# Kernel tuning notes

Measured on AMD Instinct MI355X. Metric: run time of the kernel, lower is better.

The kernel has to match this reference:

```python
import jax, jax.numpy as jnp
import numpy as np

EMBED = 1024
HEADS = 16
HDIM = 64
FF = 4096
N, S = 2, 2048
EPS = 1e-5


def _ln(x, g, b):
    m = jnp.mean(x, axis=-1, keepdims=True)
    v = jnp.mean((x - m) ** 2, axis=-1, keepdims=True)
    return (x - m) / jnp.sqrt(v + EPS) * g + b


def setup_inputs() -> dict:
    key = jax.random.key(0)
    ks = jax.random.split(key, 12)
    sd = 0.02
    inp = {
        'x': jax.random.normal(ks[0], (N, S, EMBED), dtype=jnp.float32),
        'mask': jnp.ones((N, 1, S, S), dtype=jnp.int32),
        'Wq': jax.random.normal(ks[1], (EMBED, HEADS * HDIM), dtype=jnp.float32) * sd,
        'bq': jnp.zeros((HEADS * HDIM,), dtype=jnp.float32),
        'Wk': jax.random.normal(ks[2], (EMBED, HEADS * HDIM), dtype=jnp.float32) * sd,
        'bk': jnp.zeros((HEADS * HDIM,), dtype=jnp.float32),
        'Wv': jax.random.normal(ks[3], (EMBED, HEADS * HDIM), dtype=jnp.float32) * sd,
        'bv': jnp.zeros((HEADS * HDIM,), dtype=jnp.float32),
        'Wo': jax.random.normal(ks[4], (HEADS * HDIM, EMBED), dtype=jnp.float32) * sd,
        'bo': jnp.zeros((EMBED,), dtype=jnp.float32),
        'g1': jnp.ones((EMBED,), dtype=jnp.float32),
        'beta1': jnp.zeros((EMBED,), dtype=jnp.float32),
        'g2': jnp.ones((EMBED,), dtype=jnp.float32),
        'beta2': jnp.zeros((EMBED,), dtype=jnp.float32),
        'W1': jax.random.normal(ks[5], (EMBED, FF), dtype=jnp.float32) * sd,
        'b1': jnp.zeros((FF,), dtype=jnp.float32),
        'W2': jax.random.normal(ks[6], (FF, EMBED), dtype=jnp.float32) * sd,
        'b2': jnp.zeros((EMBED,), dtype=jnp.float32),
    }
    return inp


def reference(x, mask, Wq, bq, Wk, bk, Wv, bv, Wo, bo, g1, beta1, g2, beta2, W1, b1, W2, b2):
    n, q_len, _ = x.shape
    # QKV projections, split into heads: [n, s, h, d]
    Q = (x @ Wq + bq).reshape(n, q_len, HEADS, HDIM)
    K = (x @ Wk + bk).reshape(n, q_len, HEADS, HDIM)
    V = (x @ Wv + bv).reshape(n, q_len, HEADS, HDIM)
    scores = jnp.einsum('nqhd,nkhd->nhqk', Q, K)
    scores = jnp.where(mask == 0, -jnp.inf, scores)
    # NOTE: original torch code is `attention / embed_size ** 1 / 2`,
    # which parses as (scores / embed_size) / 2 — replicated faithfully.
    attn = jax.nn.softmax(scores / EMBED / 2.0, axis=-1)
    ctx = jnp.einsum('nhqk,nkhd->nqhd', attn, V).reshape(n, q_len, HEADS * HDIM)
    proj = ctx @ Wo + bo
    h = _ln(proj + x, g1, beta1)  # dropout is identity (eval / p=0)
    ff = jax.nn.relu(h @ W1 + b1) @ W2 + b2
    out = _ln(ff + h, g2, beta2)
    return out
```

## Files before the change

kernel.cpp:

```cpp
#include <hip/hip_runtime.h>
#include <hip/hip_bf16.h>
#include <cstdint>
#include <cstddef>

#define EMBED 1024
#define SLEN  2048
#define NB    2
#define HEADS 16
#define HDIM  64
#define FFDIM 4096
#define ROWS  (NB * SLEN)
#define LOG2E 1.4426950408889634f

typedef __attribute__((ext_vector_type(8))) __bf16 bf16x8;
typedef __attribute__((ext_vector_type(4))) __bf16 bf16x4;
typedef __attribute__((ext_vector_type(4))) float  f32x4;

__device__ __forceinline__ void gload_lds16(const void* g, void* l) {
  __builtin_amdgcn_global_load_lds(
      (const __attribute__((address_space(1))) void*)g,
      (__attribute__((address_space(3))) void*)l, 16, 0, 0);
}

#define SCHED() __builtin_amdgcn_sched_barrier(0)
#define BAR()                              \
  do {                                     \
    __builtin_amdgcn_s_barrier();          \
    __builtin_amdgcn_sched_barrier(0);     \
  } while (0)
#define WAITVM(N)                                           \
  do {                                                      \
    asm volatile("s_waitcnt vmcnt(" #N ")" ::: "memory");   \
  } while (0)
#define WAITLGKM(N)                                         \
  do {                                                      \
    asm volatile("s_waitcnt lgkmcnt(" #N ")" ::: "memory"); \
  } while (0)

__global__ __launch_bounds__(256) void prologue_k(
    const float* __restrict__ x, const int* __restrict__ mask,
    const float* __restrict__ Wq, const float* __restrict__ Wk,
    const float* __restrict__ Wv, const float* __restrict__ Wo,
    const float* __restrict__ W1, const float* __restrict__ W2,
    __bf16* __restrict__ xb, int* __restrict__ flags,
    __bf16* __restrict__ Wqt, __bf16* __restrict__ Wkt, __bf16* __restrict__ Wvt,
    __bf16* __restrict__ Wot, __bf16* __restrict__ W1t, __bf16* __restrict__ W2t) {
  const int b = blockIdx.x;
  const int tid = threadIdx.x;
  if (b < 3072) {
    __shared__ float t[64][65];
    const float* src;
    __bf16* dst;
    int R, C, tile;
    if (b < 1024) {
      const int w = b >> 8;
      tile = b & 255; R = 1024; C = 1024;
      src = (w == 0) ? Wq : (w == 1) ? Wk : (w == 2) ? Wv : Wo;
      dst = (w == 0) ? Wqt : (w == 1) ? Wkt : (w == 2) ? Wvt : Wot;
    } else if (b < 2048) {
      tile = b - 1024; R = 1024; C = 4096; src = W1; dst = W1t;
    } else {
      tile = b - 2048; R = 4096; C = 1024; src = W2; dst = W2t;
    }
    const int ct = C >> 6;
    const int tr = (tile / ct) * 64, tc = (tile % ct) * 64;
    const int tx = tid & 63;
    const int ty = tid >> 6;
#pragma unroll
    for (int i = 0; i < 16; ++i) {
      int a = ty * 16 + i;
      t[a][tx] = src[(size_t)(tr + a) * C + tc + tx];
    }
    __syncthreads();
#pragma unroll
    for (int i = 0; i < 16; ++i) {
      int bb = ty * 16 + i;
      dst[(size_t)(tc + bb) * R + tr + tx] = (__bf16)t[tx][bb];
    }
  } else if (b < 4096) {
    const int base = (b - 3072) * 1024;
#pragma unroll
    for (int it = 0; it < 4; ++it) {
      const int i = base + it * 256 + tid;
      float4 v = ((const float4*)x)[i];
      bf16x4 o;
      o.x = (__bf16)v.x; o.y = (__bf16)v.y; o.z = (__bf16)v.z; o.w = (__bf16)v.w;
      ((bf16x4*)xb)[i] = o;
    }
  } else {
    const int mb = b - 4096;
    const int kt = mb & 31, qt = (mb >> 5) & 15, n = mb >> 9;
    const int* base = mask + ((size_t)n * SLEN + qt * 128) * SLEN + kt * 64;
    const int rw = tid >> 4;
    const int cg = tid & 15;
    int ok = 1;
#pragma unroll
    for (int i = 0; i < 8; ++i) {
      int4 v = ((const int4*)(base + (size_t)(rw + i * 16) * SLEN))[cg];
      ok &= (v.x != 0) & (v.y != 0) & (v.z != 0) & (v.w != 0);
    }
    __shared__ int red;
    if (tid == 0) red = 1;
    __syncthreads();
    if (!ok) red = 0;
    __syncthreads();
    if (tid == 0) flags[mb] = red;
  }
}

template <int MODE>
__global__ __launch_bounds__(512, 1) void gemm256(
    const __bf16* __restrict__ A, const __bf16* __restrict__ Bt,
    const float* __restrict__ bias, const float* __restrict__ bias2,
    const float* __restrict__ bias3,
    void* __restrict__ outp, void* __restrict__ outp2, void* __restrict__ outp3,
    int M, int N, int K, int Kc, float oscale) {
  __shared__ __align__(16) char smem[131072];
  const int tid = threadIdx.x;
  const int lane = tid & 63;
  const int ntile = N >> 8;
  const int mt = M >> 8;
  const int cpx = gridDim.x >> 3;
  int u = (blockIdx.x & 7) * cpx + (blockIdx.x >> 3);
  int kz = 0;
  if constexpr (MODE == 5) {
    const int tiles = mt * ntile;
    kz = u / tiles;
    u -= kz * tiles;
  }
  int bm, bn;
  {
    const int G = (ntile >= 4) ? 4 : ntile;
    const int gsz = mt * G;
    const int g = u / gsz;
    const int rem = u - g * gsz;
    bm = rem / G;
    bn = g * G + rem % G;
  }
  const int trow = bm << 8, tcol = bn << 8;

  const int r0 = tid & 255;
  const int c0 = tid >> 8;
  const __bf16* Ag = A + (size_t)(trow + r0) * K + (size_t)kz * Kc + c0 * 8;
  const __bf16* Bg = Bt + (size_t)(tcol + r0) * K + (size_t)kz * Kc + c0 * 8;

  auto stage = [&](int buf, int kt) {
    const __bf16* a0 = Ag + (size_t)kt * 32;
    const __bf16* b0 = Bg + (size_t)kt * 32;
    char* la = smem + buf * 32768 + tid * 16;
    char* lb = la + 16384;
    gload_lds16(a0, la);
    gload_lds16(a0 + 16, la + 8192);
    gload_lds16(b0, lb);
    gload_lds16(b0 + 16, lb + 8192);
  };

  const int wave = tid >> 6;
  const int wr = wave >> 2;
  const int wc = wave & 3;
  const int l16 = lane & 15;
  const int g4 = lane >> 4;

  f32x4 acc[8][4];
#pragma unroll
  for (int i = 0; i < 8; ++i)
#pragma unroll
    for (int j = 0; j < 4; ++j) acc[i][j] = (f32x4)0.0f;

  const int nk = Kc >> 5;
  stage(0, 0);
  stage(1, 1);
  stage(2, 2);
  WAITVM(8);
  BAR();
  for (int kt = 0; kt < nk; ++kt) {
    const int cur = kt & 3;
    const char* base = smem + cur * 32768;
    bf16x8 af[8], bfr[4];
#pragma unroll
    for (int i = 0; i < 4; ++i)
      af[i] = *(const bf16x8*)(base + g4 * 4096 + (wr * 128 + i * 16 + l16) * 16);
#pragma unroll
    for (int j = 0; j < 4; ++j)
      bfr[j] = *(const bf16x8*)(base + 16384 + g4 * 4096 + (wc * 64 + j * 16 + l16) * 16);
    SCHED();
#pragma unroll
    for (int i = 4; i < 8; ++i)
      af[i] = *(const bf16x8*)(base + g4 * 4096 + (wr * 128 + i * 16 + l16) * 16);
    if (kt + 3 < nk) stage((kt + 3) & 3, kt + 3);
    SCHED();
    WAITLGKM(4);
    SCHED();
    __builtin_amdgcn_s_setprio(1);
#pragma unroll
    for (int mi = 0; mi < 4; ++mi)
#pragma unroll
      for (int ni = 0; ni < 4; ++ni)
        acc[mi][ni] =
            __builtin_amdgcn_mfma_f32_16x16x32_bf16(af[mi], bfr[ni], acc[mi][ni], 0, 0, 0);
    __builtin_amdgcn_s_setprio(0);
    SCHED();
    WAITLGKM(0);
    SCHED();
    __builtin_amdgcn_s_setprio(1);
#pragma unroll
    for (int mi = 4; mi < 8; ++mi)
#pragma unroll
      for (int ni = 0; ni < 4; ++ni)
        acc[mi][ni] =
            __builtin_amdgcn_mfma_f32_16x16x32_bf16(af[mi], bfr[ni], acc[mi][ni], 0, 0, 0);
    __builtin_amdgcn_s_setprio(0);
    if (kt + 3 < nk) {
      WAITVM(8);
    } else if (kt + 3 == nk) {
      WAITVM(4);
    } else if (kt + 2 == nk) {
      WAITVM(0);
    }
    BAR();
  }

  if constexpr (MODE == 5) {
#pragma unroll
    for (int mi = 0; mi < 8; ++mi)
#pragma unroll
      for (int ni = 0; ni < 4; ++ni) {
        const int col = tcol + wc * 64 + ni * 16 + l16;
#pragma unroll
        for (int r = 0; r < 4; ++r) {
          const int row = trow + wr * 128 + mi * 16 + g4 * 4 + r;
          ((float*)outp)[(size_t)kz * M * N + (size_t)row * N + col] = acc[mi][ni][r];
        }
      }
  } else {
    const int sel = (MODE == 4) ? (tcol >> 10) : 0;
    const float* bp = (MODE == 4) ? (sel == 0 ? bias : sel == 1 ? bias2 : bias3) : bias;
    const int cc0 = (MODE == 4) ? (tcol & 1023) : tcol;
    const int n = trow >> 11;
    if (MODE == 4 && sel == 2) {
      __bf16(*repT)[136] = (__bf16(*)[136])smem;
#pragma unroll
      for (int h = 0; h < 2; ++h) {
        __syncthreads();
        if (wr == h) {
#pragma unroll
          for (int mi = 0; mi < 8; ++mi)
#pragma unroll
            for (int ni = 0; ni < 4; ++ni) {
              const int cl = wc * 64 + ni * 16 + l16;
              const float bcol = bp[cc0 + cl];
#pragma unroll
              for (int r = 0; r < 4; ++r)
                repT[cl][mi * 16 + g4 * 4 + r] = (__bf16)(acc[mi][ni][r] + bcol);
            }
        }
        __syncthreads();
#pragma unroll
        for (int it = 0; it < 8; ++it) {
          const int cidx = it * 512 + tid;
          const int cl = cidx >> 4, seg = cidx & 15;
          const int col = cc0 + cl, hh = col >> 6, dd = col & 63;
          *(bf16x8*)((__bf16*)outp3 + ((size_t)((n * HEADS + hh) * HDIM) + dd) * SLEN +
                     (trow & 2047) + h * 128 + seg * 8) = *(const bf16x8*)&repT[cl][seg * 8];
        }
      }
    } else {
      __bf16(*rep)[264] = (__bf16(*)[264])smem;
#pragma unroll
      for (int h = 0; h < 2; ++h) {
        __syncthreads();
        if (wr == h) {
#pragma unroll
          for (int mi = 0; mi < 8; ++mi)
#pragma unroll
            for (int ni = 0; ni < 4; ++ni) {
              const int cl = wc * 64 + ni * 16 + l16;
              float bcol = bp[cc0 + cl];
#pragma unroll
              for (int r = 0; r < 4; ++r) {
                float v = acc[mi][ni][r] + bcol;
                if constexpr (MODE == 4) {
                  if (sel == 0) v *= oscale;
                } else {
                  v = fmaxf(v, 0.0f);
                }
                rep[mi * 16 + g4 * 4 + r][cl] = (__bf16)v;
              }
            }
        }
        __syncthreads();
        if constexpr (MODE == 3) {
#pragma unroll
          for (int it = 0; it < 8; ++it) {
            const int cidx = it * 512 + tid;
            const int rl = cidx >> 5, seg = cidx & 31;
            *(bf16x8*)((__bf16*)outp + (size_t)(trow + h * 128 + rl) * N + tcol + seg * 8) =
                *(const bf16x8*)&rep[rl][seg * 8];
          }
        } else {
          __bf16* dst = (sel == 0) ? (__bf16*)outp : (__bf16*)outp2;
#pragma unroll
          for (int it = 0; it < 8; ++it) {
            const int cidx = it * 512 + tid;
            const int rl = cidx >> 5, seg = cidx & 31;
            const int col = cc0 + seg * 8, hh = col >> 6, d = col & 63;
            const int s = (trow & 2047) + h * 128 + rl;
            *(bf16x8*)(dst + ((size_t)((n * HEADS + hh) * SLEN) + s) * HDIM + d) =
                *(const bf16x8*)&rep[rl][seg * 8];
          }
        }
      }
    }
  }
}

__global__ __launch_bounds__(256, 2) void gemm_bt5(
    const __bf16* __restrict__ A, const __bf16* __restrict__ Bt,
    float* __restrict__ outp, int M, int N, int K, int Kc) {
  __shared__ __align__(16) char smem[65536];
  const int tid = threadIdx.x;
  const int lane = tid & 63;
  const int ntile = N >> 7;
  const int cpx = gridDim.x >> 3;
  int u = (blockIdx.x & 7) * cpx + (blockIdx.x >> 3);
  const int tiles = (M >> 7) * ntile;
  const int kz = u / tiles;
  u -= kz * tiles;
  const int bm = u / ntile;
  const int bn = u % ntile;
  const int trow = bm << 7;
  const int tcol = bn << 7;

  const int c0 = tid >> 7;
  const int r0 = tid & 127;
  const __bf16* Ag = A + (size_t)(trow + r0) * K + (size_t)kz * Kc + c0 * 8;
  const __bf16* Bg = Bt + (size_t)(tcol + r0) * K + (size_t)kz * Kc + c0 * 8;

  auto stage = [&](int buf, int kt) {
    const __bf16* a0 = Ag + (size_t)kt * 32;
    const __bf16* b0 = Bg + (size_t)kt * 32;
    char* la = smem + buf * 16384 + tid * 16;
    char* lb = la + 8192;
    gload_lds16(a0, la);
    gload_lds16(a0 + 16, la + 4096);
    gload_lds16(b0, lb);
    gload_lds16(b0 + 16, lb + 4096);
  };

  const int wave = tid >> 6;
  const int wr = (wave >> 1) * 64;
  const int wc = (wave & 1) * 64;
  const int l16 = lane & 15;
  const int g4 = lane >> 4;

  f32x4 acc[4][4];
#pragma unroll
  for (int i = 0; i < 4; ++i)
#pragma unroll
    for (int j = 0; j < 4; ++j) acc[i][j] = (f32x4)0.0f;

  const int nk = Kc >> 5;
  stage(0, 0);
  stage(1, 1);
  stage(2, 2);
  WAITVM(8);
  BAR();
  for (int kt = 0; kt < nk; ++kt) {
    const int cur = kt & 3;
    const char* base = smem + cur * 16384;
    bf16x8 af[4], bfr[4];
#pragma unroll
    for (int i = 0; i < 4; ++i) {
      af[i]  = *(const bf16x8*)(base + g4 * 2048 + (wr + i * 16 + l16) * 16);
      bfr[i] = *(const bf16x8*)(base + 8192 + g4 * 2048 + (wc + i * 16 + l16) * 16);
    }
    if (kt + 3 < nk) stage((kt + 3) & 3, kt + 3);
    SCHED();
    WAITLGKM(0);
    SCHED();
    __builtin_amdgcn_s_setprio(1);
#pragma unroll
    for (int mi = 0; mi < 4; ++mi)
#pragma unroll
      for (int ni = 0; ni < 4; ++ni)
        acc[mi][ni] =
            __builtin_amdgcn_mfma_f32_16x16x32_bf16(af[mi], bfr[ni], acc[mi][ni], 0, 0, 0);
    __builtin_amdgcn_s_setprio(0);
    if (kt + 3 < nk) {
      WAITVM(8);
    } else if (kt + 3 == nk) {
      WAITVM(4);
    } else if (kt + 2 == nk) {
      WAITVM(0);
    }
    BAR();
  }
#pragma unroll
  for (int mi = 0; mi < 4; ++mi)
#pragma unroll
    for (int ni = 0; ni < 4; ++ni) {
      const int col = tcol + wc + ni * 16 + l16;
#pragma unroll
      for (int r = 0; r < 4; ++r) {
        const int row = trow + wr + mi * 16 + g4 * 4 + r;
        outp[(size_t)kz * M * N + (size_t)row * N + col] = acc[mi][ni][r];
      }
    }
}

__global__ __launch_bounds__(256, 3) void attn_k(const __bf16* __restrict__ Q,
                                                 const __bf16* __restrict__ K,
                                                 const __bf16* __restrict__ Vt,
                                                 const int* __restrict__ mask,
                                                 const int* __restrict__ flags,
                                                 __bf16* __restrict__ ctx) {
  const int tid = threadIdx.x, lane = tid & 63, wave = tid >> 6;
  const int l16 = lane & 15, g4 = lane >> 4;
  const int bid = blockIdx.x;
  const int lb = (bid & 7) * 64 + (bid >> 3);
  const int qt = lb & 15, h = (lb >> 4) & 15, n = lb >> 8;
  const int q0 = qt * 128 + wave * 32;
  const __bf16* Qh = Q + (size_t)(n * HEADS + h) * SLEN * HDIM;
  const __bf16* Kh = K + (size_t)(n * HEADS + h) * SLEN * HDIM;
  const __bf16* Vh = Vt + (size_t)(n * HEADS + h) * HDIM * SLEN;
  const int* Mh = mask + (size_t)n * SLEN * SLEN;
  const int* Fh = flags + (n * 16 + qt) * 32;

  __shared__ __bf16 KV[2][2][8][64][8];
  __shared__ __align__(16) __bf16 P_lds[4][2][16][72];

  const int srow = tid & 63;
  const int schunk = tid >> 6;
  const __bf16* Kg = Kh + (size_t)srow * HDIM + schunk * 8;
  const __bf16* Vg = Vh + (size_t)srow * SLEN + schunk * 8;
  auto stage = [&](int buf, int kb) {
    char* lk = (char*)&KV[buf][0][0][0][0] + tid * 16;
    char* lv = (char*)&KV[buf][1][0][0][0] + tid * 16;
    const __bf16* kg = Kg + (size_t)kb * 64 * HDIM;
    const __bf16* vg = Vg + kb * 64;
    gload_lds16(kg, lk);
    gload_lds16(kg + 32, lk + 4096);
    gload_lds16(vg, lv);
    gload_lds16(vg + 32, lv + 4096);
  };

  const unsigned long long fbits = __ballot(Fh[lane & 31] != 0);

  bf16x8 qf[2][2];
#pragma unroll
  for (int mq = 0; mq < 2; ++mq)
#pragma unroll
    for (int kd = 0; kd < 2; ++kd)
      qf[mq][kd] =
          *(const bf16x8*)(Qh + (size_t)(q0 + mq * 16 + l16) * HDIM + kd * 32 + g4 * 8);

  float m_[2], lsum[2];
  f32x4 o[2][4];
#pragma unroll
  for (int mq = 0; mq < 2; ++mq) {
    m_[mq] = -INFINITY;
    lsum[mq] = 0.0f;
#pragma unroll
    for (int ni = 0; ni < 4; ++ni) o[mq][ni] = (f32x4)0.0f;
  }

  const int nt = SLEN / 64;
  stage(0, 0);
  stage(1, 1);
  WAITVM(4);
  BAR();
  int cur = 0;
  for (int kt = 0; kt < nt; ++kt) {
    const int kbase = kt * 64;
    const bool full = (fbits >> kt) & 1ull;
    bf16x8 kf[4][2], vf[2][4];
#pragma unroll
    for (int ni = 0; ni < 4; ++ni) {
      kf[ni][0] = *(const bf16x8*)&KV[cur][0][g4][ni * 16 + l16][0];
      kf[ni][1] = *(const bf16x8*)&KV[cur][0][4 + g4][ni * 16 + l16][0];
    }
    SCHED();
#pragma unroll
    for (int kb = 0; kb < 2; ++kb)
#pragma unroll
      for (int ni = 0; ni < 4; ++ni)
        vf[kb][ni] = *(const bf16x8*)&KV[cur][1][kb * 4 + g4][ni * 16 + l16][0];
    SCHED();
    WAITLGKM(8);
    SCHED();
    f32x4 s[2][4];
#pragma unroll
    for (int mq = 0; mq < 2; ++mq)
#pragma unroll
      for (int ni = 0; ni < 4; ++ni) s[mq][ni] = (f32x4)0.0f;
    __builtin_amdgcn_s_setprio(1);
#pragma unroll
    for (int ni = 0; ni < 4; ++ni)
#pragma unroll
      for (int mq = 0; mq < 2; ++mq) {
        s[mq][ni] = __builtin_amdgcn_mfma_f32_16x16x32_bf16(kf[ni][0], qf[mq][0], s[mq][ni], 0, 0, 0);
        s[mq][ni] = __builtin_amdgcn_mfma_f32_16x16x32_bf16(kf[ni][1], qf[mq][1], s[mq][ni], 0, 0, 0);
      }
    __builtin_amdgcn_s_setprio(0);
    if (!full) {
#pragma unroll
      for (int mq = 0; mq < 2; ++mq)
#pragma unroll
        for (int ni = 0; ni < 4; ++ni)
#pragma unroll
          for (int r = 0; r < 4; ++r) {
            const int mk =
                Mh[(size_t)(q0 + mq * 16 + l16) * SLEN + kbase + ni * 16 + 4 * g4 + r];
            s[mq][ni][r] = mk ? s[mq][ni][r] : -INFINITY;
          }
    }
    float pmax[2];
#pragma unroll
    for (int mq = 0; mq < 2; ++mq) {
      float a = fmaxf(fmaxf(s[mq][0][0], s[mq][0][1]), fmaxf(s[mq][0][2], s[mq][0][3]));
      float b = fmaxf(fmaxf(s[mq][1][0], s[mq][1][1]), fmaxf(s[mq][1][2], s[mq][1][3]));
      float c = fmaxf(fmaxf(s[mq][2][0], s[mq][2][1]), fmaxf(s[mq][2][2], s[mq][2][3]));
      float d = fmaxf(fmaxf(s[mq][3][0], s[mq][3][1]), fmaxf(s[mq][3][2], s[mq][3][3]));
      pmax[mq] = fmaxf(fmaxf(a, b), fmaxf(c, d));
    }
    const int ok = (pmax[0] <= m_[0] + 8.0f) & (pmax[1] <= m_[1] + 8.0f);
    if (!__all(ok)) {
#pragma unroll
      for (int mq = 0; mq < 2; ++mq) {
        float pm2 = fmaxf(m_[mq], pmax[mq]);
        pm2 = fmaxf(pm2, __shfl_xor(pm2, 16));
        pm2 = fmaxf(pm2, __shfl_xor(pm2, 32));
        const float al = __builtin_amdgcn_exp2f(m_[mq] - pm2);
        m_[mq] = pm2;
        lsum[mq] *= al;
#pragma unroll
        for (int r = 0; r < 4; ++r) {
          const float ao = __shfl(al, 4 * g4 + r);
#pragma unroll
          for (int ni = 0; ni < 4; ++ni) o[mq][ni][r] *= ao;
        }
      }
    }
#pragma unroll
    for (int mq = 0; mq < 2; ++mq) {
      float ls = 0.0f;
#pragma unroll
      for (int ni = 0; ni < 4; ++ni) {
        bf16x4 pk;
#pragma unroll
        for (int r = 0; r < 4; ++r) {
          const float p = __builtin_amdgcn_exp2f(s[mq][ni][r] - m_[mq]);
          ls += p;
          pk[r] = (__bf16)p;
        }
        *(bf16x4*)&P_lds[wave][mq][l16][ni * 16 + 4 * g4] = pk;
      }
      lsum[mq] += ls;
    }
    bf16x8 pa[2][2];
#pragma unroll
    for (int kb = 0; kb < 2; ++kb) {
      pa[0][kb] = *(const bf16x8*)&P_lds[wave][0][l16][kb * 32 + 8 * g4];
      pa[1][kb] = *(const bf16x8*)&P_lds[wave][1][l16][kb * 32 + 8 * g4];
    }
    SCHED();
    WAITLGKM(0);
    SCHED();
    __builtin_amdgcn_s_setprio(1);
#pragma unroll
    for (int kb = 0; kb < 2; ++kb)
#pragma unroll
      for (int ni = 0; ni < 4; ++ni) {
        o[0][ni] = __builtin_amdgcn_mfma_f32_16x16x32_bf16(pa[0][kb], vf[kb][ni], o[0][ni], 0, 0, 0);
        o[1][ni] = __builtin_amdgcn_mfma_f32_16x16x32_bf16(pa[1][kb], vf[kb][ni], o[1][ni], 0, 0, 0);
      }
    __builtin_amdgcn_s_setprio(0);
    WAITVM(0);
    BAR();
    if (kt + 2 < nt) stage(cur, kt + 2);
    cur ^= 1;
  }
#pragma unroll
  for (int mq = 0; mq < 2; ++mq) {
    float l = lsum[mq];
    l += __shfl_xor(l, 16);
    l += __shfl_xor(l, 32);
    lsum[mq] = l;
  }
#pragma unroll
  for (int mq = 0; mq < 2; ++mq) {
#pragma unroll
    for (int r = 0; r < 4; ++r) {
      const float inv = __builtin_amdgcn_rcpf(__shfl(lsum[mq], 4 * g4 + r));
#pragma unroll
      for (int ni = 0; ni < 4; ++ni) {
        ctx[((size_t)(n * SLEN) + q0 + mq * 16 + 4 * g4 + r) * EMBED + h * HDIM + ni * 16 +
            l16] = (__bf16)(o[mq][ni][r] * inv);
      }
    }
  }
}

__global__ __launch_bounds__(256) void ln_fused_k(const float* __restrict__ p, int nz,
                                                  const float* __restrict__ bias,
                                                  const float* __restrict__ res,
                                                  const float* __restrict__ gw,
                                                  const float* __restrict__ bw,
                                                  float* __restrict__ of,
                                                  __bf16* __restrict__ ob) {
  const int tid = threadIdx.x;
  const size_t row = blockIdx.x;
  float4 bb = ((const float4*)bias)[tid];
  float4 rr = ((const float4*)(res + row * EMBED))[tid];
  float4 v;
  v.x = bb.x + rr.x; v.y = bb.y + rr.y; v.z = bb.z + rr.z; v.w = bb.w + rr.w;
  for (int z = 0; z < nz; ++z) {
    float4 pz = ((const float4*)(p + (size_t)z * ROWS * EMBED + row * EMBED))[tid];
    v.x += pz.x; v.y += pz.y; v.z += pz.z; v.w += pz.w;
  }
  float s = v.x + v.y + v.z + v.w;
  float sq = v.x * v.x + v.y * v.y + v.z * v.z + v.w * v.w;
#pragma unroll
  for (int off = 1; off < 64; off <<= 1) {
    s += __shfl_xor(s, off);
    sq += __shfl_xor(sq, off);
  }
  __shared__ float red[8];
  if ((tid & 63) == 0) { red[tid >> 6] = s; red[4 + (tid >> 6)] = sq; }
  __syncthreads();
  s = red[0] + red[1] + red[2] + red[3];
  sq = red[4] + red[5] + red[6] + red[7];
  const float mean = s * (1.0f / EMBED);
  const float var = sq * (1.0f / EMBED) - mean * mean;
  const float rstd = rsqrtf(var + 1e-5f);
  float4 gv = ((const float4*)gw)[tid];
  float4 bv2 = ((const float4*)bw)[tid];
  float4 ov;
  ov.x = (v.x - mean) * rstd * gv.x + bv2.x;
  ov.y = (v.y - mean) * rstd * gv.y + bv2.y;
  ov.z = (v.z - mean) * rstd * gv.z + bv2.z;
  ov.w = (v.w - mean) * rstd * gv.w + bv2.w;
  ((float4*)(of + row * EMBED))[tid] = ov;
  if (ob) {
    bf16x4 oh;
    oh.x = (__bf16)ov.x; oh.y = (__bf16)ov.y; oh.z = (__bf16)ov.z; oh.w = (__bf16)ov.w;
    ((bf16x4*)(ob + row * EMBED))[tid] = oh;
  }
}

extern "C" void kernel_launch(void* const* d_in, const int* in_sizes, int n_in,
                              void* d_out, int out_size, void* d_ws, size_t ws_size,
                              hipStream_t stream) {
  (void)in_sizes; (void)n_in; (void)out_size;
  const float* x   = (const float*)d_in[0];
  const int*  mask = (const int*)d_in[1];
  const float* Wq = (const float*)d_in[2];  const float* bq  = (const float*)d_in[3];
  const float* Wk = (const float*)d_in[4];  const float* bk  = (const float*)d_in[5];
  const float* Wv = (const float*)d_in[6];  const float* bv  = (const float*)d_in[7];
  const float* Wo = (const float*)d_in[8];  const float* bo  = (const float*)d_in[9];
  const float* g1 = (const float*)d_in[10]; const float* be1 = (const float*)d_in[11];
  const float* g2 = (const float*)d_in[12]; const float* be2 = (const float*)d_in[13];
  const float* W1 = (const float*)d_in[14]; const float* b1  = (const float*)d_in[15];
  const float* W2 = (const float*)d_in[16]; const float* b2  = (const float*)d_in[17];

  char* ws = (char*)d_ws;
  size_t off = 0;
  auto alloc = [&](size_t bytes) -> void* {
    void* p = ws + off;
    off += (bytes + 255) & ~(size_t)255;
    return p;
  };
  __bf16* xb   = (__bf16*)alloc((size_t)ROWS * EMBED * 2);
  __bf16* Wqt  = (__bf16*)alloc((size_t)EMBED * EMBED * 2);
  __bf16* Wkt  = (__bf16*)alloc((size_t)EMBED * EMBED * 2);
  __bf16* Wvt  = (__bf16*)alloc((size_t)EMBED * EMBED * 2);
  __bf16* Wot  = (__bf16*)alloc((size_t)EMBED * EMBED * 2);
  __bf16* W1t  = (__bf16*)alloc((size_t)EMBED * FFDIM * 2);
  __bf16* W2t  = (__bf16*)alloc((size_t)FFDIM * EMBED * 2);
  __bf16* Qb   = (__bf16*)alloc((size_t)ROWS * EMBED * 2);
  __bf16* Kb   = (__bf16*)alloc((size_t)ROWS * EMBED * 2);
  __bf16* Vtb  = (__bf16*)alloc((size_t)ROWS * EMBED * 2);
  __bf16* ctxb = (__bf16*)alloc((size_t)ROWS * EMBED * 2);
  float* hf     = (float*)alloc((size_t)ROWS * EMBED * 4);
  __bf16* hb    = (__bf16*)alloc((size_t)ROWS * EMBED * 2);
  __bf16* a1    = (__bf16*)alloc((size_t)ROWS * FFDIM * 2);
  int*   mflags = (int*)alloc(NB * 16 * 32 * sizeof(int));

  const size_t pneed = (size_t)4 * ROWS * EMBED * sizeof(float);
  int kspF2;
  float* pF2;
  if (off + pneed <= ws_size) {
    pF2 = (float*)alloc(pneed);
    kspF2 = 4;
  } else {
    pF2 = (float*)Qb;
    kspF2 = 2;
  }
  float* pWo = (float*)a1;

  prologue_k<<<5120, 256, 0, stream>>>(x, mask, Wq, Wk, Wv, Wo, W1, W2,
                                       xb, mflags, Wqt, Wkt, Wvt, Wot, W1t, W2t);

  gemm256<4><<<(ROWS / 256) * (3 * EMBED / 256), 512, 0, stream>>>(
      xb, Wqt, bq, bk, bv, Qb, Kb, Vtb, ROWS, 3 * EMBED, EMBED, EMBED, LOG2E / 2048.0f);
  attn_k<<<NB * HEADS * (SLEN / 128), 256, 0, stream>>>(Qb, Kb, Vtb, mask, mflags, ctxb);
  gemm_bt5<<<(ROWS / 128) * (EMBED / 128) * 2, 256, 0, stream>>>(
      ctxb, Wot, pWo, ROWS, EMBED, EMBED, EMBED / 2);
  ln_fused_k<<<ROWS, 256, 0, stream>>>(pWo, 2, bo, x, g1, be1, hf, hb);
  gemm256<3><<<(ROWS / 256) * (FFDIM / 256), 512, 0, stream>>>(
      hb, W1t, b1, nullptr, nullptr, a1, nullptr, nullptr, ROWS, FFDIM, EMBED, EMBED, 1.0f);
  gemm256<5><<<(ROWS / 256) * (EMBED / 256) * kspF2, 512, 0, stream>>>(
      a1, W2t, nullptr, nullptr, nullptr, pF2, nullptr, nullptr,
      ROWS, EMBED, FFDIM, FFDIM / kspF2, 1.0f);
  ln_fused_k<<<ROWS, 256, 0, stream>>>(pF2, kspF2, b2, hf, g2, be2, (float*)d_out, nullptr);
}
```

Baseline: 284.5 us.

## Split attention work across 8 waves with 16 query rows per wave

```diff
diff --git a/kernel.cpp b/kernel.cpp
--- a/kernel.cpp
+++ b/kernel.cpp
@@ -408,7 +408,7 @@
     }
 }
 
-__global__ __launch_bounds__(256, 3) void attn_k(const __bf16* __restrict__ Q,
+__global__ __launch_bounds__(512, 2) void attn_k(const __bf16* __restrict__ Q,
                                                  const __bf16* __restrict__ K,
                                                  const __bf16* __restrict__ Vt,
                                                  const int* __restrict__ mask,
@@ -419,7 +419,7 @@
   const int bid = blockIdx.x;
   const int lb = (bid & 7) * 64 + (bid >> 3);
   const int qt = lb & 15, h = (lb >> 4) & 15, n = lb >> 8;
-  const int q0 = qt * 128 + wave * 32;
+  const int q0 = qt * 128 + wave * 16;
   const __bf16* Qh = Q + (size_t)(n * HEADS + h) * SLEN * HDIM;
   const __bf16* Kh = K + (size_t)(n * HEADS + h) * SLEN * HDIM;
   const __bf16* Vh = Vt + (size_t)(n * HEADS + h) * HDIM * SLEN;
@@ -427,7 +427,7 @@
   const int* Fh = flags + (n * 16 + qt) * 32;
 
   __shared__ __bf16 KV[2][2][8][64][8];
-  __shared__ __align__(16) __bf16 P_lds[4][2][16][72];
+  __shared__ __align__(16) __bf16 P_lds[8][16][72];
 
   const int srow = tid & 63;
   const int schunk = tid >> 6;
@@ -436,38 +436,26 @@
   auto stage = [&](int buf, int kb) {
     char* lk = (char*)&KV[buf][0][0][0][0] + tid * 16;
     char* lv = (char*)&KV[buf][1][0][0][0] + tid * 16;
-    const __bf16* kg = Kg + (size_t)kb * 64 * HDIM;
-    const __bf16* vg = Vg + kb * 64;
-    gload_lds16(kg, lk);
-    gload_lds16(kg + 32, lk + 4096);
-    gload_lds16(vg, lv);
-    gload_lds16(vg + 32, lv + 4096);
+    gload_lds16(Kg + (size_t)kb * 64 * HDIM, lk);
+    gload_lds16(Vg + kb * 64, lv);
   };
 
   const unsigned long long fbits = __ballot(Fh[lane & 31] != 0);
 
-  bf16x8 qf[2][2];
-#pragma unroll
-  for (int mq = 0; mq < 2; ++mq)
-#pragma unroll
-    for (int kd = 0; kd < 2; ++kd)
-      qf[mq][kd] =
-          *(const bf16x8*)(Qh + (size_t)(q0 + mq * 16 + l16) * HDIM + kd * 32 + g4 * 8);
-
-  float m_[2], lsum[2];
-  f32x4 o[2][4];
-#pragma unroll
-  for (int mq = 0; mq < 2; ++mq) {
-    m_[mq] = -INFINITY;
-    lsum[mq] = 0.0f;
-#pragma unroll
-    for (int ni = 0; ni < 4; ++ni) o[mq][ni] = (f32x4)0.0f;
-  }
+  bf16x8 qf[2];
+#pragma unroll
+  for (int kd = 0; kd < 2; ++kd)
+    qf[kd] = *(const bf16x8*)(Qh + (size_t)(q0 + l16) * HDIM + kd * 32 + g4 * 8);
+
+  float m_ = -INFINITY, lsum = 0.0f;
+  f32x4 o[4];
+#pragma unroll
+  for (int ni = 0; ni < 4; ++ni) o[ni] = (f32x4)0.0f;
 
   const int nt = SLEN / 64;
   stage(0, 0);
   stage(1, 1);
-  WAITVM(4);
+  WAITVM(2);
   BAR();
   int cur = 0;
   for (int kt = 0; kt < nt; ++kt) {
@@ -488,81 +476,61 @@
     SCHED();
     WAITLGKM(8);
     SCHED();
-    f32x4 s[2][4];
-#pragma unroll
-    for (int mq = 0; mq < 2; ++mq)
-#pragma unroll
-      for (int ni = 0; ni < 4; ++ni) s[mq][ni] = (f32x4)0.0f;
+    f32x4 s[4];
+#pragma unroll
+    for (int ni = 0; ni < 4; ++ni) s[ni] = (f32x4)0.0f;
     __builtin_amdgcn_s_setprio(1);
 #pragma unroll
-    for (int ni = 0; ni < 4; ++ni)
-#pragma unroll
-      for (int mq = 0; mq < 2; ++mq) {
-        s[mq][ni] = __builtin_amdgcn_mfma_f32_16x16x32_bf16(kf[ni][0], qf[mq][0], s[mq][ni], 0, 0, 0);
-        s[mq][ni] = __builtin_amdgcn_mfma_f32_16x16x32_bf16(kf[ni][1], qf[mq][1], s[mq][ni], 0, 0, 0);
-      }
+    for (int ni = 0; ni < 4; ++ni) {
+      s[ni] = __builtin_amdgcn_mfma_f32_16x16x32_bf16(kf[ni][0], qf[0], s[ni], 0, 0, 0);
+      s[ni] = __builtin_amdgcn_mfma_f32_16x16x32_bf16(kf[ni][1], qf[1], s[ni], 0, 0, 0);
+    }
     __builtin_amdgcn_s_setprio(0);
     if (!full) {
 #pragma unroll
-      for (int mq = 0; mq < 2; ++mq)
-#pragma unroll
-        for (int ni = 0; ni < 4; ++ni)
-#pragma unroll
-          for (int r = 0; r < 4; ++r) {
-            const int mk =
-                Mh[(size_t)(q0 + mq * 16 + l16) * SLEN + kbase + ni * 16 + 4 * g4 + r];
-            s[mq][ni][r] = mk ? s[mq][ni][r] : -INFINITY;
-          }
-    }
-    float pmax[2];
-#pragma unroll
-    for (int mq = 0; mq < 2; ++mq) {
-      float a = fmaxf(fmaxf(s[mq][0][0], s[mq][0][1]), fmaxf(s[mq][0][2], s[mq][0][3]));
-      float b = fmaxf(fmaxf(s[mq][1][0], s[mq][1][1]), fmaxf(s[mq][1][2], s[mq][1][3]));
-      float c = fmaxf(fmaxf(s[mq][2][0], s[mq][2][1]), fmaxf(s[mq][2][2], s[mq][2][3]));
-      float d = fmaxf(fmaxf(s[mq][3][0], s[mq][3][1]), fmaxf(s[mq][3][2], s[mq][3][3]));
-      pmax[mq] = fmaxf(fmaxf(a, b), fmaxf(c, d));
-    }
-    const int ok = (pmax[0] <= m_[0] + 8.0f) & (pmax[1] <= m_[1] + 8.0f);
-    if (!__all(ok)) {
-#pragma unroll
-      for (int mq = 0; mq < 2; ++mq) {
-        float pm2 = fmaxf(m_[mq], pmax[mq]);
-        pm2 = fmaxf(pm2, __shfl_xor(pm2, 16));
-        pm2 = fmaxf(pm2, __shfl_xor(pm2, 32));
-        const float al = __builtin_amdgcn_exp2f(m_[mq] - pm2);
-        m_[mq] = pm2;
-        lsum[mq] *= al;
+      for (int ni = 0; ni < 4; ++ni)
 #pragma unroll
         for (int r = 0; r < 4; ++r) {
-          const float ao = __shfl(al, 4 * g4 + r);
-#pragma unroll
-          for (int ni = 0; ni < 4; ++ni) o[mq][ni][r] *= ao;
+          const int mk = Mh[(size_t)(q0 + l16) * SLEN + kbase + ni * 16 + 4 * g4 + r];
+          s[ni][r] = mk ? s[ni][r] : -INFINITY;
         }
+    }
+    float a = fmaxf(fmaxf(s[0][0], s[0][1]), fmaxf(s[0][2], s[0][3]));
+    float b = fmaxf(fmaxf(s[1][0], s[1][1]), fmaxf(s[1][2], s[1][3]));
+    float c = fmaxf(fmaxf(s[2][0], s[2][1]), fmaxf(s[2][2], s[2][3]));
+    float d = fmaxf(fmaxf(s[3][0], s[3][1]), fmaxf(s[3][2], s[3][3]));
+    const float pmax = fmaxf(fmaxf(a, b), fmaxf(c, d));
+    if (!__all(pmax <= m_ + 8.0f)) {
+      float pm2 = fmaxf(m_, pmax);
+      pm2 = fmaxf(pm2, __shfl_xor(pm2, 16));
+      pm2 = fmaxf(pm2, __shfl_xor(pm2, 32));
+      const float al = __builtin_amdgcn_exp2f(m_ - pm2);
+      m_ = pm2;
+      lsum *= al;
+#pragma unroll
+      for (int r = 0; r < 4; ++r) {
+        const float ao = __shfl(al, 4 * g4 + r);
+#pragma unroll
+        for (int ni = 0; ni < 4; ++ni) o[ni][r] *= ao;
       }
     }
-#pragma unroll
-    for (int mq = 0; mq < 2; ++mq) {
-      float ls = 0.0f;
-#pragma unroll
-      for (int ni = 0; ni < 4; ++ni) {
-        bf16x4 pk;
-#pragma unroll
-        for (int r = 0; r < 4; ++r) {
-          const float p = __builtin_amdgcn_exp2f(s[mq][ni][r] - m_[mq]);
-          ls += p;
-          pk[r] = (__bf16)p;
-        }
-        *(bf16x4*)&P_lds[wave][mq][l16][ni * 16 + 4 * g4] = pk;
+    float ls = 0.0f;
+#pragma unroll
+    for (int ni = 0; ni < 4; ++ni) {
+      bf16x4 pk;
+#pragma unroll
+      for (int r = 0; r < 4; ++r) {
+        const float p = __builtin_amdgcn_exp2f(s[ni][r] - m_);
+        ls += p;
+        pk[r] = (__bf16)p;
       }
-      lsum[mq] += ls;
-    }
-    bf16x8 pa[2][2];
-#pragma unroll
-    for (int kb = 0; kb < 2; ++kb) {
-      pa[0][kb] = *(const bf16x8*)&P_lds[wave][0][l16][kb * 32 + 8 * g4];
-      pa[1][kb] = *(const bf16x8*)&P_lds[wave][1][l16][kb * 32 + 8 * g4];
-    }
+      *(bf16x4*)&P_lds[wave][l16][ni * 16 + 4 * g4] = pk;
+    }
+    lsum += ls;
+    bf16x8 pa[2];
+#pragma unroll
+    for (int kb = 0; kb < 2; ++kb)
+      pa[kb] = *(const bf16x8*)&P_lds[wave][l16][kb * 32 + 8 * g4];
     SCHED();
     WAITLGKM(0);
     SCHED();
@@ -570,33 +538,27 @@
 #pragma unroll
     for (int kb = 0; kb < 2; ++kb)
 #pragma unroll
-      for (int ni = 0; ni < 4; ++ni) {
-        o[0][ni] = __builtin_amdgcn_mfma_f32_16x16x32_bf16(pa[0][kb], vf[kb][ni], o[0][ni], 0, 0, 0);
-        o[1][ni] = __builtin_amdgcn_mfma_f32_16x16x32_bf16(pa[1][kb], vf[kb][ni], o[1][ni], 0, 0, 0);
-      }
+      for (int ni = 0; ni < 4; ++ni)
+        o[ni] = __builtin_amdgcn_mfma_f32_16x16x32_bf16(pa[kb], vf[kb][ni], o[ni], 0, 0, 0);
     __builtin_amdgcn_s_setprio(0);
     WAITVM(0);
     BAR();
     if (kt + 2 < nt) stage(cur, kt + 2);
     cur ^= 1;
   }
-#pragma unroll
-  for (int mq = 0; mq < 2; ++mq) {
-    float l = lsum[mq];
+  {
+    float l = lsum;
     l += __shfl_xor(l, 16);
     l += __shfl_xor(l, 32);
-    lsum[mq] = l;
-  }
-#pragma unroll
-  for (int mq = 0; mq < 2; ++mq) {
-#pragma unroll
-    for (int r = 0; r < 4; ++r) {
-      const float inv = __builtin_amdgcn_rcpf(__shfl(lsum[mq], 4 * g4 + r));
-#pragma unroll
-      for (int ni = 0; ni < 4; ++ni) {
-        ctx[((size_t)(n * SLEN) + q0 + mq * 16 + 4 * g4 + r) * EMBED + h * HDIM + ni * 16 +
-            l16] = (__bf16)(o[mq][ni][r] * inv);
-      }
+    lsum = l;
+  }
+#pragma unroll
+  for (int r = 0; r < 4; ++r) {
+    const float inv = __builtin_amdgcn_rcpf(__shfl(lsum, 4 * g4 + r));
+#pragma unroll
+    for (int ni = 0; ni < 4; ++ni) {
+      ctx[((size_t)(n * SLEN) + q0 + 4 * g4 + r) * EMBED + h * HDIM + ni * 16 + l16] =
+          (__bf16)(o[ni][r] * inv);
     }
   }
 }
@@ -703,7 +665,7 @@
 
   gemm256<4><<<(ROWS / 256) * (3 * EMBED / 256), 512, 0, stream>>>(
       xb, Wqt, bq, bk, bv, Qb, Kb, Vtb, ROWS, 3 * EMBED, EMBED, EMBED, LOG2E / 2048.0f);
-  attn_k<<<NB * HEADS * (SLEN / 128), 256, 0, stream>>>(Qb, Kb, Vtb, mask, mflags, ctxb);
+  attn_k<<<NB * HEADS * (SLEN / 128), 512, 0, stream>>>(Qb, Kb, Vtb, mask, mflags, ctxb);
   gemm_bt5<<<(ROWS / 128) * (EMBED / 128) * 2, 256, 0, stream>>>(
       ctxb, Wot, pWo, ROWS, EMBED, EMBED, EMBED / 2);
   ln_fused_k<<<ROWS, 256, 0, stream>>>(pWo, 2, bo, x, g1, be1, hf, hb);
```

After: 277.3 us. -2.5%, faster.
